# Performance work log

Measured on AMD Instinct MI355X. Metric: run time of the kernel, lower is better.

Reference implementation:

```python
import jax, jax.numpy as jnp
import numpy as np

INPUT_SIZE = 512
UNITS = 1024


def setup_inputs() -> dict:
    key = jax.random.key(0)
    k_x, k_wih, k_whh, k_bih, k_bhh = jax.random.split(key, 5)
    B, T = 128, 512
    s_ih = 1.0 / np.sqrt(UNITS)
    return {
        "inputs": jax.random.normal(k_x, (B, T, INPUT_SIZE), dtype=jnp.float32),
        # torch nn.LSTMCell params: gate order i, f, g, o
        "W_ih": jax.random.uniform(k_wih, (4 * UNITS, INPUT_SIZE), minval=-s_ih, maxval=s_ih, dtype=jnp.float32),
        "W_hh": jax.random.uniform(k_whh, (4 * UNITS, UNITS), minval=-s_ih, maxval=s_ih, dtype=jnp.float32),
        "b_ih": jax.random.uniform(k_bih, (4 * UNITS,), minval=-s_ih, maxval=s_ih, dtype=jnp.float32),
        "b_hh": jax.random.uniform(k_bhh, (4 * UNITS,), minval=-s_ih, maxval=s_ih, dtype=jnp.float32),
    }


def reference(inputs, W_ih, W_hh, b_ih, b_hh):
    B, T, _ = inputs.shape
    U = W_hh.shape[1]
    # Precompute input contribution for all timesteps: [B, T, 4U]
    x_gates = jnp.einsum('bti,gi->btg', inputs, W_ih) + b_ih + b_hh

    def step(carry, xg):
        h, c = carry
        gates = xg + h @ W_hh.T  # [B, 4U]
        i, f, g, o = jnp.split(gates, 4, axis=-1)
        i = jax.nn.sigmoid(i)
        f = jax.nn.sigmoid(f)
        g = jnp.tanh(g)
        o = jax.nn.sigmoid(o)
        c = f * c + i * g
        h = o * jnp.tanh(c)
        return (h, c), h

    h0 = jnp.zeros((B, U), dtype=inputs.dtype)
    c0 = jnp.zeros((B, U), dtype=inputs.dtype)
    _, hs = jax.lax.scan(step, (h0, c0), jnp.swapaxes(x_gates, 0, 1))
    return jnp.swapaxes(hs, 0, 1)  # [B, T, U] (return_sequences=True)
```

## Files before the change

### kernel.cpp

```cpp
#include <hip/hip_runtime.h>
#include <hip/hip_bf16.h>

typedef __attribute__((ext_vector_type(8))) short short8;
typedef __attribute__((ext_vector_type(4))) float f32x4;
typedef unsigned int u32;
typedef unsigned short u16;

#define T_STEPS 512
#define B_SZ    128
#define I_SZ    512
#define U_SZ    1024
#define K_TOT   1536

#define XB_OFF   0
#define WC_OFF   67108864
#define FLAG_OFF 79691776
#define HBUF_OFF 79708160

__device__ __forceinline__ u16 f2bf(float f) {
  u32 u = __float_as_uint(f);
  u32 r = (u + 0x7fffu + ((u >> 16) & 1u)) >> 16;
  return (u16)r;
}

__device__ __forceinline__ float sigm(float x) { return 1.f / (1.f + __expf(-x)); }
__device__ __forceinline__ float tanh_s(float x) {
  float ax = fabsf(x);
  float e  = __expf(-2.f * ax);
  float t  = (1.f - e) / (1.f + e);
  return copysignf(t, x);
}

__global__ void k_convX(const float* __restrict__ X, u16* __restrict__ Xb) {
  u32 i = blockIdx.x * 256u + threadIdx.x;
  float4 v = reinterpret_cast<const float4*>(X)[i];
  uint2 o;
  o.x = (u32)f2bf(v.x) | ((u32)f2bf(v.y) << 16);
  o.y = (u32)f2bf(v.z) | ((u32)f2bf(v.w) << 16);
  reinterpret_cast<uint2*>(Xb)[i] = o;
}

__global__ void k_packW(const float* __restrict__ Wih, const float* __restrict__ Whh,
                        u16* __restrict__ Wc) {
  const int gcol = blockIdx.x;
  for (int k = threadIdx.x; k < K_TOT; k += 256) {
    float v = (k < I_SZ) ? Wih[(size_t)gcol * I_SZ + k]
                         : Whh[(size_t)gcol * U_SZ + (k - I_SZ)];
    Wc[(size_t)gcol * K_TOT + k] = f2bf(v);
  }
}

__global__ void k_zero(u32* __restrict__ hz, u32* __restrict__ flags) {
  u32 i = blockIdx.x * 256u + threadIdx.x;
  if (i < 131072u) hz[i] = 0u;
  else             flags[i - 131072u] = 0u;
}

__device__ __forceinline__ short8 load_b128_bypass(const u16* p) {
  short8 r;
  asm volatile("global_load_dwordx4 %0, %1, off sc0 sc1" : "=v"(r) : "v"(p));
  return r;
}
__device__ __forceinline__ void store_b16_bypass(u16* p, u32 v) {
  asm volatile("global_store_short %0, %1, off sc0 sc1" :: "v"(p), "v"(v));
}

__device__ __forceinline__ void poll_flags(const u32* flags, u32 tgt, int lane) {
  for (;;) {
    u32 a = __hip_atomic_load(flags + lane,       __ATOMIC_RELAXED, __HIP_MEMORY_SCOPE_AGENT);
    u32 b = __hip_atomic_load(flags + lane + 64,  __ATOMIC_RELAXED, __HIP_MEMORY_SCOPE_AGENT);
    u32 c = __hip_atomic_load(flags + lane + 128, __ATOMIC_RELAXED, __HIP_MEMORY_SCOPE_AGENT);
    u32 d = __hip_atomic_load(flags + lane + 192, __ATOMIC_RELAXED, __HIP_MEMORY_SCOPE_AGENT);
    bool ok = (a >= tgt) & (b >= tgt) & (c >= tgt) & (d >= tgt);
    if (__all((int)ok)) return;
    __builtin_amdgcn_s_sleep(1);
  }
}

__global__ __launch_bounds__(512, 2)
void lstm_scan(const u16* __restrict__ Xb, const u16* __restrict__ Wc,
               const float* __restrict__ bih, const float* __restrict__ bhh,
               u16* __restrict__ hbuf, u32* __restrict__ flags,
               float* __restrict__ out) {
  __shared__ __align__(16) float gbuf[8][64][36];

  const int tid  = threadIdx.x;
  const int wg   = blockIdx.x;
  const int cl   = wg >> 6;
  const int wloc = wg & 63;
  const int rb   = cl * 32;
  const int u0   = wloc * 16;
  const int wid  = tid >> 6;
  const int lane = tid & 63;
  const int l15  = lane & 15;
  const int kg   = lane >> 4;
  const int kw   = wid;

  short8 Bf[6][4];
  #pragma unroll
  for (int ct = 0; ct < 4; ++ct) {
    const int gcol = ct * 1024 + u0 + l15;
    const u16* wrow = Wc + (size_t)gcol * K_TOT;
    #pragma unroll
    for (int i = 0; i < 6; ++i) {
      const int k = (i * 8 + kw) * 32 + kg * 8;
      Bf[i][ct] = *reinterpret_cast<const short8*>(wrow + k);
    }
  }

  const int b_l = tid >> 4;
  const int uu  = tid & 15;
  float bsum[4];
  #pragma unroll
  for (int g = 0; g < 4; ++g)
    bsum[g] = bih[g * 1024 + u0 + uu] + bhh[g * 1024 + u0 + uu];
  float c_state = 0.f;
  float* orow = out + (size_t)(rb + b_l) * (T_STEPS * U_SZ) + u0 + uu;
  const int hidx = (rb + b_l) * U_SZ + u0 + uu;

  const int r0 = rb + l15;
  const int r1 = r0 + 16;
  const u16* xrow0 = Xb + (size_t)r0 * (T_STEPS * I_SZ);
  const u16* xrow1 = Xb + (size_t)r1 * (T_STEPS * I_SZ);

  for (int t = 0; t < T_STEPS; ++t) {
    const u16* hsrc = hbuf + ((t & 1) ^ 1) * (B_SZ * U_SZ);
    u16*       hdst = hbuf + (t & 1) * (B_SZ * U_SZ);
    const u16* px0 = xrow0 + (size_t)t * I_SZ;
    const u16* px1 = xrow1 + (size_t)t * I_SZ;

    f32x4 acc[2][4];
    #pragma unroll
    for (int rt = 0; rt < 2; ++rt)
      #pragma unroll
      for (int ct = 0; ct < 4; ++ct)
        acc[rt][ct] = (f32x4){0.f, 0.f, 0.f, 0.f};

    #pragma unroll
    for (int i = 0; i < 2; ++i) {
      const int k = (i * 8 + kw) * 32 + kg * 8;
      const short8 a0 = *reinterpret_cast<const short8*>(px0 + k);
      const short8 a1 = *reinterpret_cast<const short8*>(px1 + k);
      #pragma unroll
      for (int ct = 0; ct < 4; ++ct) {
        acc[0][ct] = __builtin_amdgcn_mfma_f32_16x16x32_bf16(a0, Bf[i][ct], acc[0][ct], 0, 0, 0);
        acc[1][ct] = __builtin_amdgcn_mfma_f32_16x16x32_bf16(a1, Bf[i][ct], acc[1][ct], 0, 0, 0);
      }
    }

    if (tid < 64) poll_flags(flags, (u32)t, lane);
    __syncthreads();

    short8 hA[4][2];
    #pragma unroll
    for (int ih = 0; ih < 4; ++ih) {
      const int ku = (ih * 8 + kw) * 32 + kg * 8;
      hA[ih][0] = load_b128_bypass(hsrc + (size_t)r0 * U_SZ + ku);
      hA[ih][1] = load_b128_bypass(hsrc + (size_t)r1 * U_SZ + ku);
    }
    asm volatile("s_waitcnt vmcnt(0)" ::: "memory");
    __builtin_amdgcn_sched_barrier(0);
    #pragma unroll
    for (int ih = 0; ih < 4; ++ih)
      #pragma unroll
      for (int ct = 0; ct < 4; ++ct) {
        acc[0][ct] = __builtin_amdgcn_mfma_f32_16x16x32_bf16(hA[ih][0], Bf[2 + ih][ct], acc[0][ct], 0, 0, 0);
        acc[1][ct] = __builtin_amdgcn_mfma_f32_16x16x32_bf16(hA[ih][1], Bf[2 + ih][ct], acc[1][ct], 0, 0, 0);
      }

    #pragma unroll
    for (int rt = 0; rt < 2; ++rt)
      #pragma unroll
      for (int ct = 0; ct < 4; ++ct)
        *reinterpret_cast<float4*>(&gbuf[kw][ct * 16 + l15][rt * 16 + kg * 4]) =
            *reinterpret_cast<float4*>(&acc[rt][ct]);
    __syncthreads();

    float gs[4];
    #pragma unroll
    for (int g = 0; g < 4; ++g) {
      float s = bsum[g];
      #pragma unroll
      for (int k2 = 0; k2 < 8; ++k2) s += gbuf[k2][g * 16 + uu][b_l];
      gs[g] = s;
    }
    const float ig = sigm(gs[0]);
    const float fg = sigm(gs[1]);
    const float gg = tanh_s(gs[2]);
    const float og = sigm(gs[3]);
    c_state = fg * c_state + ig * gg;
    const float h = og * tanh_s(c_state);

    orow[(size_t)t * U_SZ] = h;
    store_b16_bypass(hdst + hidx, (u32)f2bf(h));

    asm volatile("s_waitcnt vmcnt(0)" ::: "memory");
    __syncthreads();
    if (tid == 0)
      __hip_atomic_store(flags + wg, (u32)(t + 1), __ATOMIC_RELAXED, __HIP_MEMORY_SCOPE_AGENT);
  }
}

extern "C" void kernel_launch(void* const* d_in, const int* in_sizes, int n_in,
                              void* d_out, int out_size, void* d_ws, size_t ws_size,
                              hipStream_t stream) {
  const float* X   = (const float*)d_in[0];
  const float* Wih = (const float*)d_in[1];
  const float* Whh = (const float*)d_in[2];
  const float* bih = (const float*)d_in[3];
  const float* bhh = (const float*)d_in[4];
  float* out = (float*)d_out;
  char*  ws  = (char*)d_ws;

  u16* Xb    = (u16*)(ws + XB_OFF);
  u16* Wc    = (u16*)(ws + WC_OFF);
  u32* flags = (u32*)(ws + FLAG_OFF);
  u16* hbuf  = (u16*)(ws + HBUF_OFF);

  hipLaunchKernelGGL(k_convX, dim3(32768), dim3(256), 0, stream, X, Xb);
  hipLaunchKernelGGL(k_packW, dim3(4096), dim3(256), 0, stream, Wih, Whh, Wc);
  hipLaunchKernelGGL(k_zero,  dim3(513),  dim3(256), 0, stream, (u32*)hbuf, flags);

  void* args[] = {(void*)&Xb, (void*)&Wc, (void*)&bih, (void*)&bhh,
                  (void*)&hbuf, (void*)&flags, (void*)&out};
  hipLaunchCooperativeKernel((void*)lstm_scan, dim3(256), dim3(512), args, 0, stream);
}
```

Measured before the change: 2.605 ms.

## Repartition LSTM scan into 8 independent batch clusters with LDS-staged h

Result: slower. 3.375 ms (+29.5%).

```diff
diff --git a/kernel.cpp b/kernel.cpp
--- a/kernel.cpp
+++ b/kernel.cpp
@@ -22,7 +22,6 @@
   u32 r = (u + 0x7fffu + ((u >> 16) & 1u)) >> 16;
   return (u16)r;
 }
-
 __device__ __forceinline__ float sigm(float x) { return 1.f / (1.f + __expf(-x)); }
 __device__ __forceinline__ float tanh_s(float x) {
   float ax = fabsf(x);
@@ -52,29 +51,17 @@
 
 __global__ void k_zero(u32* __restrict__ hz, u32* __restrict__ flags) {
   u32 i = blockIdx.x * 256u + threadIdx.x;
-  if (i < 131072u) hz[i] = 0u;
-  else             flags[i - 131072u] = 0u;
-}
-
-__device__ __forceinline__ short8 load_b128_bypass(const u16* p) {
+  if (i < 131072u)      hz[i] = 0u;
+  else if (i < 131328u) flags[i - 131072u] = 0u;
+}
+
+__device__ __forceinline__ short8 ld_h16(const u16* p) {
   short8 r;
   asm volatile("global_load_dwordx4 %0, %1, off sc0 sc1" : "=v"(r) : "v"(p));
   return r;
 }
-__device__ __forceinline__ void store_b16_bypass(u16* p, u32 v) {
-  asm volatile("global_store_short %0, %1, off sc0 sc1" :: "v"(p), "v"(v));
-}
-
-__device__ __forceinline__ void poll_flags(const u32* flags, u32 tgt, int lane) {
-  for (;;) {
-    u32 a = __hip_atomic_load(flags + lane,       __ATOMIC_RELAXED, __HIP_MEMORY_SCOPE_AGENT);
-    u32 b = __hip_atomic_load(flags + lane + 64,  __ATOMIC_RELAXED, __HIP_MEMORY_SCOPE_AGENT);
-    u32 c = __hip_atomic_load(flags + lane + 128, __ATOMIC_RELAXED, __HIP_MEMORY_SCOPE_AGENT);
-    u32 d = __hip_atomic_load(flags + lane + 192, __ATOMIC_RELAXED, __HIP_MEMORY_SCOPE_AGENT);
-    bool ok = (a >= tgt) & (b >= tgt) & (c >= tgt) & (d >= tgt);
-    if (__all((int)ok)) return;
-    __builtin_amdgcn_s_sleep(1);
-  }
+__device__ __forceinline__ void st_h(u16* p, u32 v) {
+  asm volatile("global_store_short %0, %1, off sc0 sc1" :: "v"(p), "v"(v) : "memory");
 }
 
 __global__ __launch_bounds__(512, 2)
@@ -82,107 +69,123 @@
                const float* __restrict__ bih, const float* __restrict__ bhh,
                u16* __restrict__ hbuf, u32* __restrict__ flags,
                float* __restrict__ out) {
-  __shared__ __align__(16) float gbuf[8][64][36];
+  __shared__ __align__(16) char hst[32768];
+  __shared__ __align__(16) float gbuf[2][128][20];
 
   const int tid  = threadIdx.x;
   const int wg   = blockIdx.x;
-  const int cl   = wg >> 6;
-  const int wloc = wg & 63;
-  const int rb   = cl * 32;
-  const int u0   = wloc * 16;
+  const int cl   = wg >> 5;
+  const int wloc = wg & 31;
+  const int u0   = wloc * 32;
   const int wid  = tid >> 6;
   const int lane = tid & 63;
   const int l15  = lane & 15;
   const int kg   = lane >> 4;
-  const int kw   = wid;
-
-  short8 Bf[6][4];
+  const int cw   = wid >> 1;
+  const int kq   = wid & 1;
+  const int swzr = (l15 & 7) << 4;
+
+  short8 Bf_x[8][2], Bf_h[16][2];
   #pragma unroll
-  for (int ct = 0; ct < 4; ++ct) {
-    const int gcol = ct * 1024 + u0 + l15;
+  for (int cf = 0; cf < 2; ++cf) {
+    const int lc   = cw * 32 + cf * 16 + l15;
+    const int gcol = (lc >> 5) * 1024 + u0 + (lc & 31);
     const u16* wrow = Wc + (size_t)gcol * K_TOT;
     #pragma unroll
-    for (int i = 0; i < 6; ++i) {
-      const int k = (i * 8 + kw) * 32 + kg * 8;
-      Bf[i][ct] = *reinterpret_cast<const short8*>(wrow + k);
+    for (int i = 0; i < 8; ++i) {
+      const int k = (i * 2 + kq) * 32 + kg * 8;
+      Bf_x[i][cf] = *reinterpret_cast<const short8*>(wrow + k);
+    }
+    #pragma unroll
+    for (int ih = 0; ih < 16; ++ih) {
+      const int k = ((8 + ih) * 2 + kq) * 32 + kg * 8;
+      Bf_h[ih][cf] = *reinterpret_cast<const short8*>(wrow + k);
     }
   }
 
-  const int b_l = tid >> 4;
-  const int uu  = tid & 15;
+  const int row  = tid >> 5;
+  const int uloc = tid & 31;
+  const int ug   = u0 + uloc;
   float bsum[4];
   #pragma unroll
-  for (int g = 0; g < 4; ++g)
-    bsum[g] = bih[g * 1024 + u0 + uu] + bhh[g * 1024 + u0 + uu];
+  for (int g = 0; g < 4; ++g) bsum[g] = bih[g * 1024 + ug] + bhh[g * 1024 + ug];
   float c_state = 0.f;
-  float* orow = out + (size_t)(rb + b_l) * (T_STEPS * U_SZ) + u0 + uu;
-  const int hidx = (rb + b_l) * U_SZ + u0 + uu;
-
-  const int r0 = rb + l15;
-  const int r1 = r0 + 16;
-  const u16* xrow0 = Xb + (size_t)r0 * (T_STEPS * I_SZ);
-  const u16* xrow1 = Xb + (size_t)r1 * (T_STEPS * I_SZ);
+  const int rowg = cl * 16 + row;
+  float* orow = out + (size_t)rowg * (T_STEPS * U_SZ) + ug;
+  u16* hb_cl  = hbuf + cl * 32768;
+  u32* myflag = flags + (cl << 5) + wloc;
+  u32* pollp  = flags + (cl << 5) + (lane & 31);
+
+  const u16* xrow = Xb + ((size_t)(cl * 16 + l15)) * (T_STEPS * I_SZ);
 
   for (int t = 0; t < T_STEPS; ++t) {
-    const u16* hsrc = hbuf + ((t & 1) ^ 1) * (B_SZ * U_SZ);
-    u16*       hdst = hbuf + (t & 1) * (B_SZ * U_SZ);
-    const u16* px0 = xrow0 + (size_t)t * I_SZ;
-    const u16* px1 = xrow1 + (size_t)t * I_SZ;
-
-    f32x4 acc[2][4];
-    #pragma unroll
-    for (int rt = 0; rt < 2; ++rt)
+    const u16* hsrc = hb_cl + ((t & 1) ^ 1) * 16384;
+    u16*       hdst = hb_cl + (t & 1) * 16384;
+    const u16* px   = xrow + (size_t)t * I_SZ;
+
+    f32x4 acc[2];
+    acc[0] = (f32x4){0.f, 0.f, 0.f, 0.f};
+    acc[1] = (f32x4){0.f, 0.f, 0.f, 0.f};
+
+    #pragma unroll
+    for (int i = 0; i < 8; ++i) {
+      const int k = (i * 2 + kq) * 32 + kg * 8;
+      const short8 a = *reinterpret_cast<const short8*>(px + k);
       #pragma unroll
-      for (int ct = 0; ct < 4; ++ct)
-        acc[rt][ct] = (f32x4){0.f, 0.f, 0.f, 0.f};
-
-    #pragma unroll
-    for (int i = 0; i < 2; ++i) {
-      const int k = (i * 8 + kw) * 32 + kg * 8;
-      const short8 a0 = *reinterpret_cast<const short8*>(px0 + k);
-      const short8 a1 = *reinterpret_cast<const short8*>(px1 + k);
+      for (int cf = 0; cf < 2; ++cf)
+        acc[cf] = __builtin_amdgcn_mfma_f32_16x16x32_bf16(a, Bf_x[i][cf], acc[cf], 0, 0, 0);
+    }
+
+    if (tid < 64) {
+      for (;;) {
+        const u32 v = __hip_atomic_load(pollp, __ATOMIC_RELAXED, __HIP_MEMORY_SCOPE_AGENT);
+        const bool ok = (lane < 32) ? (v >= (u32)t) : true;
+        if (__all((int)ok)) break;
+        __builtin_amdgcn_s_sleep(1);
+      }
+    }
+    __syncthreads();
+
+    short8 hv[4];
+    #pragma unroll
+    for (int j = 0; j < 4; ++j) {
+      const int c  = j * 512 + tid;
+      const int hr = c & 15;
+      const int k8 = c >> 4;
+      hv[j] = ld_h16(hsrc + hr * 1024 + k8 * 8);
+    }
+    asm volatile("s_waitcnt vmcnt(0)" ::: "memory");
+    #pragma unroll
+    for (int j = 0; j < 4; ++j) {
+      const int c  = j * 512 + tid;
+      const int hr = c & 15;
+      const int k8 = c >> 4;
+      *reinterpret_cast<short8*>(hst + ((hr * 2048 + k8 * 16) ^ ((hr & 7) << 4))) = hv[j];
+    }
+    __syncthreads();
+
+    #pragma unroll
+    for (int ih = 0; ih < 16; ++ih) {
+      const int kb = ((8 + ih) * 2 + kq) * 64 + kg * 16 - 1024;
+      const short8 a = *reinterpret_cast<const short8*>(hst + ((l15 * 2048 + kb) ^ swzr));
       #pragma unroll
-      for (int ct = 0; ct < 4; ++ct) {
-        acc[0][ct] = __builtin_amdgcn_mfma_f32_16x16x32_bf16(a0, Bf[i][ct], acc[0][ct], 0, 0, 0);
-        acc[1][ct] = __builtin_amdgcn_mfma_f32_16x16x32_bf16(a1, Bf[i][ct], acc[1][ct], 0, 0, 0);
-      }
-    }
-
-    if (tid < 64) poll_flags(flags, (u32)t, lane);
-    __syncthreads();
-
-    short8 hA[4][2];
-    #pragma unroll
-    for (int ih = 0; ih < 4; ++ih) {
-      const int ku = (ih * 8 + kw) * 32 + kg * 8;
-      hA[ih][0] = load_b128_bypass(hsrc + (size_t)r0 * U_SZ + ku);
-      hA[ih][1] = load_b128_bypass(hsrc + (size_t)r1 * U_SZ + ku);
-    }
-    asm volatile("s_waitcnt vmcnt(0)" ::: "memory");
-    __builtin_amdgcn_sched_barrier(0);
-    #pragma unroll
-    for (int ih = 0; ih < 4; ++ih)
-      #pragma unroll
-      for (int ct = 0; ct < 4; ++ct) {
-        acc[0][ct] = __builtin_amdgcn_mfma_f32_16x16x32_bf16(hA[ih][0], Bf[2 + ih][ct], acc[0][ct], 0, 0, 0);
-        acc[1][ct] = __builtin_amdgcn_mfma_f32_16x16x32_bf16(hA[ih][1], Bf[2 + ih][ct], acc[1][ct], 0, 0, 0);
-      }
-
-    #pragma unroll
-    for (int rt = 0; rt < 2; ++rt)
-      #pragma unroll
-      for (int ct = 0; ct < 4; ++ct)
-        *reinterpret_cast<float4*>(&gbuf[kw][ct * 16 + l15][rt * 16 + kg * 4]) =
-            *reinterpret_cast<float4*>(&acc[rt][ct]);
+      for (int cf = 0; cf < 2; ++cf)
+        acc[cf] = __builtin_amdgcn_mfma_f32_16x16x32_bf16(a, Bf_h[ih][cf], acc[cf], 0, 0, 0);
+    }
+
+    #pragma unroll
+    for (int cf = 0; cf < 2; ++cf) {
+      const int lc = cw * 32 + cf * 16 + l15;
+      *reinterpret_cast<float4*>(&gbuf[kq][lc][kg * 4]) =
+          *reinterpret_cast<float4*>(&acc[cf]);
+    }
     __syncthreads();
 
     float gs[4];
     #pragma unroll
     for (int g = 0; g < 4; ++g) {
-      float s = bsum[g];
-      #pragma unroll
-      for (int k2 = 0; k2 < 8; ++k2) s += gbuf[k2][g * 16 + uu][b_l];
-      gs[g] = s;
+      const int col = g * 32 + uloc;
+      gs[g] = bsum[g] + gbuf[0][col][row] + gbuf[1][col][row];
     }
     const float ig = sigm(gs[0]);
     const float fg = sigm(gs[1]);
@@ -192,12 +195,12 @@
     const float h = og * tanh_s(c_state);
 
     orow[(size_t)t * U_SZ] = h;
-    store_b16_bypass(hdst + hidx, (u32)f2bf(h));
+    st_h(hdst + row * 1024 + ug, (u32)f2bf(h));
 
     asm volatile("s_waitcnt vmcnt(0)" ::: "memory");
     __syncthreads();
     if (tid == 0)
-      __hip_atomic_store(flags + wg, (u32)(t + 1), __ATOMIC_RELAXED, __HIP_MEMORY_SCOPE_AGENT);
+      __hip_atomic_store(myflag, (u32)(t + 1), __ATOMIC_RELAXED, __HIP_MEMORY_SCOPE_AGENT);
   }
 }
 
```

## Restrict step sync to per-cluster flags, poll per wave, defer output store

Applied to the files above, without the earlier changes.

Result: no change. 2.584 ms (-0.8%).

```diff
diff --git a/kernel.cpp b/kernel.cpp
--- a/kernel.cpp
+++ b/kernel.cpp
@@ -22,7 +22,6 @@
   u32 r = (u + 0x7fffu + ((u >> 16) & 1u)) >> 16;
   return (u16)r;
 }
-
 __device__ __forceinline__ float sigm(float x) { return 1.f / (1.f + __expf(-x)); }
 __device__ __forceinline__ float tanh_s(float x) {
   float ax = fabsf(x);
@@ -52,29 +51,22 @@
 
 __global__ void k_zero(u32* __restrict__ hz, u32* __restrict__ flags) {
   u32 i = blockIdx.x * 256u + threadIdx.x;
-  if (i < 131072u) hz[i] = 0u;
-  else             flags[i - 131072u] = 0u;
-}
-
-__device__ __forceinline__ short8 load_b128_bypass(const u16* p) {
+  if (i < 131072u)      hz[i] = 0u;
+  else if (i < 131328u) flags[i - 131072u] = 0u;
+}
+
+__device__ __forceinline__ short8 ld_h16(const u16* p) {
   short8 r;
   asm volatile("global_load_dwordx4 %0, %1, off sc0 sc1" : "=v"(r) : "v"(p));
   return r;
 }
-__device__ __forceinline__ void store_b16_bypass(u16* p, u32 v) {
-  asm volatile("global_store_short %0, %1, off sc0 sc1" :: "v"(p), "v"(v));
-}
-
-__device__ __forceinline__ void poll_flags(const u32* flags, u32 tgt, int lane) {
-  for (;;) {
-    u32 a = __hip_atomic_load(flags + lane,       __ATOMIC_RELAXED, __HIP_MEMORY_SCOPE_AGENT);
-    u32 b = __hip_atomic_load(flags + lane + 64,  __ATOMIC_RELAXED, __HIP_MEMORY_SCOPE_AGENT);
-    u32 c = __hip_atomic_load(flags + lane + 128, __ATOMIC_RELAXED, __HIP_MEMORY_SCOPE_AGENT);
-    u32 d = __hip_atomic_load(flags + lane + 192, __ATOMIC_RELAXED, __HIP_MEMORY_SCOPE_AGENT);
-    bool ok = (a >= tgt) & (b >= tgt) & (c >= tgt) & (d >= tgt);
-    if (__all((int)ok)) return;
-    __builtin_amdgcn_s_sleep(1);
-  }
+__device__ __forceinline__ void st_h(u16* p, u32 v) {
+  asm volatile("global_store_short %0, %1, off sc0 sc1" :: "v"(p), "v"(v) : "memory");
+}
+__device__ __forceinline__ short8 ld_w16(const u16* p) {
+  short8 r;
+  asm volatile("global_load_dwordx4 %0, %1, off" : "=v"(r) : "v"(p));
+  return r;
 }
 
 __global__ __launch_bounds__(512, 2)
@@ -104,19 +96,23 @@
     #pragma unroll
     for (int i = 0; i < 6; ++i) {
       const int k = (i * 8 + kw) * 32 + kg * 8;
-      Bf[i][ct] = *reinterpret_cast<const short8*>(wrow + k);
+      Bf[i][ct] = ld_w16(wrow + k);
     }
   }
+  asm volatile("s_waitcnt vmcnt(0)" ::: "memory");
+  __builtin_amdgcn_sched_barrier(0);
 
   const int b_l = tid >> 4;
   const int uu  = tid & 15;
+  const int ug  = u0 + uu;
   float bsum[4];
   #pragma unroll
-  for (int g = 0; g < 4; ++g)
-    bsum[g] = bih[g * 1024 + u0 + uu] + bhh[g * 1024 + u0 + uu];
+  for (int g = 0; g < 4; ++g) bsum[g] = bih[g * 1024 + ug] + bhh[g * 1024 + ug];
   float c_state = 0.f;
-  float* orow = out + (size_t)(rb + b_l) * (T_STEPS * U_SZ) + u0 + uu;
-  const int hidx = (rb + b_l) * U_SZ + u0 + uu;
+  float* orow = out + (size_t)(rb + b_l) * (T_STEPS * U_SZ) + ug;
+  const int hidx = (rb + b_l) * U_SZ + ug;
+  u32* myflag = flags + (cl << 6) + wloc;
+  u32* pollp  = flags + (cl << 6) + lane;
 
   const int r0 = rb + l15;
   const int r1 = r0 + 16;
@@ -148,15 +144,18 @@
       }
     }
 
-    if (tid < 64) poll_flags(flags, (u32)t, lane);
-    __syncthreads();
+    for (;;) {
+      const u32 v = __hip_atomic_load(pollp, __ATOMIC_RELAXED, __HIP_MEMORY_SCOPE_AGENT);
+      if (__all((int)(v >= (u32)t))) break;
+      __builtin_amdgcn_s_sleep(1);
+    }
 
     short8 hA[4][2];
     #pragma unroll
     for (int ih = 0; ih < 4; ++ih) {
-      const int ku = (ih * 8 + kw) * 32 + kg * 8;
-      hA[ih][0] = load_b128_bypass(hsrc + (size_t)r0 * U_SZ + ku);
-      hA[ih][1] = load_b128_bypass(hsrc + (size_t)r1 * U_SZ + ku);
+      const int ku = ((2 + ih) * 8 + kw) * 32 + kg * 8 - 512;
+      hA[ih][0] = ld_h16(hsrc + (size_t)r0 * U_SZ + ku);
+      hA[ih][1] = ld_h16(hsrc + (size_t)r1 * U_SZ + ku);
     }
     asm volatile("s_waitcnt vmcnt(0)" ::: "memory");
     __builtin_amdgcn_sched_barrier(0);
@@ -191,13 +190,13 @@
     c_state = fg * c_state + ig * gg;
     const float h = og * tanh_s(c_state);
 
-    orow[(size_t)t * U_SZ] = h;
-    store_b16_bypass(hdst + hidx, (u32)f2bf(h));
-
+    st_h(hdst + hidx, (u32)f2bf(h));
     asm volatile("s_waitcnt vmcnt(0)" ::: "memory");
     __syncthreads();
     if (tid == 0)
-      __hip_atomic_store(flags + wg, (u32)(t + 1), __ATOMIC_RELAXED, __HIP_MEMORY_SCOPE_AGENT);
+      __hip_atomic_store(myflag, (u32)(t + 1), __ATOMIC_RELAXED, __HIP_MEMORY_SCOPE_AGENT);
+
+    orow[(size_t)t * U_SZ] = h;
   }
 }
 
```
